# Performance work log

Measured on AMD Instinct MI355X. Metric: run time of the kernel, lower is better.

Reference implementation:

```python
import jax, jax.numpy as jnp
import numpy as np

B, T, F = 8, 8192, 1024
H, O = 256, 2


def setup_inputs() -> dict:
    key = jax.random.key(0)
    ks = jax.random.split(key, 12)
    s = 0.02
    return {
        "bags": jax.random.normal(ks[0], (B, T, F), dtype=jnp.float32),
        "mask": jnp.zeros((B, T), dtype=bool),
        "W1": jax.random.normal(ks[1], (F, H), dtype=jnp.float32) * s,
        "b1": jnp.zeros((H,), dtype=jnp.float32),
        "Wv": jax.random.normal(ks[2], (H, H), dtype=jnp.float32) * s,
        "bv": jnp.zeros((H,), dtype=jnp.float32),
        "Wu": jax.random.normal(ks[3], (H, H), dtype=jnp.float32) * s,
        "bu": jnp.zeros((H,), dtype=jnp.float32),
        "ww": jax.random.normal(ks[4], (H, 1), dtype=jnp.float32) * s,
        "bw": jnp.zeros((1,), dtype=jnp.float32),
        "Wc": jax.random.normal(ks[5], (H, O), dtype=jnp.float32) * s,
        "bc": jnp.zeros((O,), dtype=jnp.float32),
    }


def reference(bags, mask, W1, b1, Wv, bv, Wu, bu, ww, bw, Wc, bc):
    # Feature projection + ReLU (dropout is identity in eval mode)
    h = jax.nn.relu(jnp.einsum("btf,fh->bth", bags, W1) + b1)  # (B,T,H)
    # Gated attention
    a_v = jnp.tanh(jnp.einsum("bth,hk->btk", h, Wv) + bv)
    a_u = jax.nn.sigmoid(jnp.einsum("bth,hk->btk", h, Wu) + bu)
    attn_logits = (jnp.einsum("bth,ho->bto", a_v * a_u, ww) + bw)[..., 0]  # (B,T)
    attn_logits = jnp.where(mask, -jnp.inf, attn_logits)
    attn = jax.nn.softmax(attn_logits, axis=1)  # (B,T)
    # Weighted aggregation over tiles
    slide_repr = jnp.einsum("bt,bth->bh", attn, h)  # (B,H)
    logits = slide_repr @ Wc + bc  # (B,O)
    return logits
```

## Files before the change

### kernel.cpp

```cpp
#include <hip/hip_runtime.h>
#include <math.h>

#define BB 8
#define TT 8192
#define FF 1024
#define HH 256
#define OO 2
#define MT 64
#define NBLK ((BB*TT)/MT)
#define PBAG (TT/MT)
#define PSTR 260

typedef __attribute__((ext_vector_type(8))) short bf16x8;
typedef __attribute__((ext_vector_type(4))) float f32x4;

__device__ __forceinline__ float b2f(unsigned short s) {
    union { unsigned u; float f; } v; v.u = ((unsigned)s) << 16; return v.f;
}
__device__ __forceinline__ unsigned short f2b(float f) {
    union { float f; unsigned u; } v; v.f = f;
    unsigned u = v.u;
    return (unsigned short)((u + 0x7fffu + ((u >> 16) & 1u)) >> 16);
}

__global__ void mil_prep(const float* __restrict__ W1,
                         const float* __restrict__ Wv,
                         const float* __restrict__ Wu,
                         unsigned short* __restrict__ W1t,
                         unsigned short* __restrict__ Wvt,
                         unsigned short* __restrict__ Wut) {
    int i = blockIdx.x;
    int t = threadIdx.x;
    if (i < 1024) {
        W1t[t * 1024 + i] = f2b(W1[i * 256 + t]);
    } else if (i < 1280) {
        int r = i - 1024;
        Wvt[t * 256 + r] = f2b(Wv[r * 256 + t]);
    } else {
        int r = i - 1280;
        Wut[t * 256 + r] = f2b(Wu[r * 256 + t]);
    }
}

__global__ __launch_bounds__(256, 2)
void mil_main(const float* __restrict__ bags,
              const unsigned char* __restrict__ mask,
              const float* __restrict__ b1,
              const float* __restrict__ bv,
              const float* __restrict__ bu,
              const float* __restrict__ ww,
              const float* __restrict__ bwp,
              const unsigned short* __restrict__ W1t,
              const unsigned short* __restrict__ Wvt,
              const unsigned short* __restrict__ Wut,
              float* __restrict__ P) {
    const int tid  = threadIdx.x;
    const int wave = tid >> 6;
    const int lane = tid & 63;
    const int l15  = lane & 15;
    const int quad = lane >> 4;
    const int blk  = blockIdx.x;
    const int row0 = blk * MT;
    const int bag  = blk >> 7;
    const int trow = (blk & 127) * MT;

    __shared__ unsigned short As[MT * 72];
    __shared__ unsigned short Bs[HH * 72];
    __shared__ unsigned short Hs[MT * 264];

    const float bwv = bwp[0];

    f32x4 acc[4][4];
#pragma unroll
    for (int mi = 0; mi < 4; ++mi)
#pragma unroll
        for (int ni = 0; ni < 4; ++ni)
            acc[mi][ni] = (f32x4){0.f, 0.f, 0.f, 0.f};

    const float* bagrow = bags + (size_t)row0 * FF;

    for (int kb = 0; kb < FF / 64; ++kb) {
        __syncthreads();
#pragma unroll
        for (int i = 0; i < 4; ++i) {
            int f = tid + i * 256;
            int r = f >> 4, s = f & 15;
            const float4 v = *(const float4*)(bagrow + (size_t)r * FF + kb * 64 + s * 4);
            unsigned p0 = (unsigned)f2b(v.x) | ((unsigned)f2b(v.y) << 16);
            unsigned p1 = (unsigned)f2b(v.z) | ((unsigned)f2b(v.w) << 16);
            *(uint2*)&As[r * 72 + s * 4] = make_uint2(p0, p1);
        }
#pragma unroll
        for (int i = 0; i < 8; ++i) {
            int f = tid + i * 256;
            int n = f >> 3, s = f & 7;
            *(uint4*)&Bs[n * 72 + s * 8] = *(const uint4*)(W1t + n * 1024 + kb * 64 + s * 8);
        }
        __syncthreads();
#pragma unroll
        for (int k0 = 0; k0 < 64; k0 += 32) {
            bf16x8 af[4], bfr[4];
#pragma unroll
            for (int mi = 0; mi < 4; ++mi)
                af[mi] = *(const bf16x8*)&As[(mi * 16 + l15) * 72 + k0 + quad * 8];
#pragma unroll
            for (int ni = 0; ni < 4; ++ni)
                bfr[ni] = *(const bf16x8*)&Bs[(wave * 64 + ni * 16 + l15) * 72 + k0 + quad * 8];
#pragma unroll
            for (int mi = 0; mi < 4; ++mi)
#pragma unroll
                for (int ni = 0; ni < 4; ++ni)
                    acc[mi][ni] = __builtin_amdgcn_mfma_f32_16x16x32_bf16(af[mi], bfr[ni], acc[mi][ni], 0, 0, 0);
        }
    }

    {
        float bb[4];
#pragma unroll
        for (int ni = 0; ni < 4; ++ni) bb[ni] = b1[wave * 64 + ni * 16 + l15];
#pragma unroll
        for (int mi = 0; mi < 4; ++mi)
#pragma unroll
            for (int ni = 0; ni < 4; ++ni) {
                int n = wave * 64 + ni * 16 + l15;
#pragma unroll
                for (int r = 0; r < 4; ++r) {
                    int m = mi * 16 + quad * 4 + r;
                    float h = acc[mi][ni][r] + bb[ni];
                    h = fmaxf(h, 0.f);
                    Hs[m * 264 + n] = f2b(h);
                }
            }
    }
    __syncthreads();

    float* logits = (float*)As;
    float* wrow   = logits + 64;
    float* sc     = wrow + 64;
    if (tid < MT) logits[tid] = 0.f;

    float gv[4][4][4];
    float rsum[4][4];
#pragma unroll
    for (int mi = 0; mi < 4; ++mi)
#pragma unroll
        for (int r = 0; r < 4; ++r) rsum[mi][r] = 0.f;

    for (int pass = 0; pass < 2; ++pass) {
        const unsigned short* Wt = pass ? Wut : Wvt;
        f32x4 a2[4][4];
#pragma unroll
        for (int mi = 0; mi < 4; ++mi)
#pragma unroll
            for (int ni = 0; ni < 4; ++ni) a2[mi][ni] = (f32x4){0.f, 0.f, 0.f, 0.f};

        for (int kb = 0; kb < HH / 64; ++kb) {
            __syncthreads();
#pragma unroll
            for (int i = 0; i < 8; ++i) {
                int f = tid + i * 256;
                int n = f >> 3, s = f & 7;
                *(uint4*)&Bs[n * 72 + s * 8] = *(const uint4*)(Wt + n * 256 + kb * 64 + s * 8);
            }
            __syncthreads();
#pragma unroll
            for (int k0 = 0; k0 < 64; k0 += 32) {
                int k = kb * 64 + k0 + quad * 8;
                bf16x8 af[4], bfr[4];
#pragma unroll
                for (int mi = 0; mi < 4; ++mi)
                    af[mi] = *(const bf16x8*)&Hs[(mi * 16 + l15) * 264 + k];
#pragma unroll
                for (int ni = 0; ni < 4; ++ni)
                    bfr[ni] = *(const bf16x8*)&Bs[(wave * 64 + ni * 16 + l15) * 72 + k0 + quad * 8];
#pragma unroll
                for (int mi = 0; mi < 4; ++mi)
#pragma unroll
                    for (int ni = 0; ni < 4; ++ni)
                        a2[mi][ni] = __builtin_amdgcn_mfma_f32_16x16x32_bf16(af[mi], bfr[ni], a2[mi][ni], 0, 0, 0);
            }
        }

        if (pass == 0) {
            float bb[4];
#pragma unroll
            for (int ni = 0; ni < 4; ++ni) bb[ni] = bv[wave * 64 + ni * 16 + l15];
#pragma unroll
            for (int mi = 0; mi < 4; ++mi)
#pragma unroll
                for (int ni = 0; ni < 4; ++ni)
#pragma unroll
                    for (int r = 0; r < 4; ++r)
                        gv[mi][ni][r] = tanhf(a2[mi][ni][r] + bb[ni]);
        } else {
            float bb[4], wn[4];
#pragma unroll
            for (int ni = 0; ni < 4; ++ni) {
                int n = wave * 64 + ni * 16 + l15;
                bb[ni] = bu[n];
                wn[ni] = ww[n];
            }
#pragma unroll
            for (int mi = 0; mi < 4; ++mi)
#pragma unroll
                for (int ni = 0; ni < 4; ++ni)
#pragma unroll
                    for (int r = 0; r < 4; ++r) {
                        float su = 1.f / (1.f + expf(-(a2[mi][ni][r] + bb[ni])));
                        rsum[mi][r] += gv[mi][ni][r] * su * wn[ni];
                    }
#pragma unroll
            for (int mi = 0; mi < 4; ++mi)
#pragma unroll
                for (int r = 0; r < 4; ++r) {
                    float s = rsum[mi][r];
                    s += __shfl_xor(s, 1);
                    s += __shfl_xor(s, 2);
                    s += __shfl_xor(s, 4);
                    s += __shfl_xor(s, 8);
                    if (l15 == 0) atomicAdd(&logits[mi * 16 + quad * 4 + r], s);
                }
        }
    }
    __syncthreads();

    if (tid < MT) {
        float lg = logits[tid] + bwv;
        if (mask[bag * TT + trow + tid]) lg = -INFINITY;
        logits[tid] = lg;
    }
    __syncthreads();

    if (wave == 0) {
        float v = logits[lane];
        float mx = v;
#pragma unroll
        for (int off = 1; off < 64; off <<= 1) mx = fmaxf(mx, __shfl_xor(mx, off));
        float w = (mx == -INFINITY) ? 0.f : expf(v - mx);
        wrow[lane] = w;
        float l = w;
#pragma unroll
        for (int off = 1; off < 64; off <<= 1) l += __shfl_xor(l, off);
        if (lane == 0) { sc[0] = mx; sc[1] = l; }
    }
    __syncthreads();

    float a = 0.f;
#pragma unroll 8
    for (int m = 0; m < MT; ++m)
        a += wrow[m] * b2f(Hs[m * 264 + tid]);

    float* rec = P + (size_t)blk * PSTR;
    rec[2 + tid] = a;
    if (tid == 0) { rec[0] = sc[0]; rec[1] = sc[1]; }
}

__global__ void mil_final(const float* __restrict__ P,
                          const float* __restrict__ Wc,
                          const float* __restrict__ bc,
                          float* __restrict__ out) {
    const int bag = blockIdx.x;
    const int tid = threadIdx.x;
    __shared__ float marr[PBAG];
    __shared__ float earr[PBAG];
    __shared__ float slide[HH];
    __shared__ float wred[8];
    __shared__ float sM, sL;

    if (tid < PBAG) marr[tid] = P[(size_t)(bag * PBAG + tid) * PSTR + 0];
    __syncthreads();
    if (tid == 0) {
        float M = -INFINITY;
        for (int i = 0; i < PBAG; ++i) M = fmaxf(M, marr[i]);
        sM = M;
    }
    __syncthreads();
    const float M = sM;
    if (tid < PBAG) {
        float e = (marr[tid] == -INFINITY) ? 0.f : expf(marr[tid] - M);
        earr[tid] = e;
        marr[tid] = P[(size_t)(bag * PBAG + tid) * PSTR + 1] * e;
    }
    __syncthreads();
    if (tid == 0) {
        float L = 0.f;
        for (int i = 0; i < PBAG; ++i) L += marr[i];
        sL = L;
    }
    __syncthreads();
    const float L = sL;

    float accv = 0.f;
    for (int i = 0; i < PBAG; ++i)
        accv += earr[i] * P[(size_t)(bag * PBAG + i) * PSTR + 2 + tid];
    slide[tid] = accv / L;
    __syncthreads();

    float p0 = slide[tid] * Wc[tid * 2 + 0];
    float p1 = slide[tid] * Wc[tid * 2 + 1];
#pragma unroll
    for (int off = 1; off < 64; off <<= 1) {
        p0 += __shfl_xor(p0, off);
        p1 += __shfl_xor(p1, off);
    }
    if ((tid & 63) == 0) {
        wred[(tid >> 6) * 2 + 0] = p0;
        wred[(tid >> 6) * 2 + 1] = p1;
    }
    __syncthreads();
    if (tid == 0) {
        out[bag * 2 + 0] = wred[0] + wred[2] + wred[4] + wred[6] + bc[0];
        out[bag * 2 + 1] = wred[1] + wred[3] + wred[5] + wred[7] + bc[1];
    }
}

extern "C" void kernel_launch(void* const* d_in, const int* in_sizes, int n_in,
                              void* d_out, int out_size, void* d_ws, size_t ws_size,
                              hipStream_t stream) {
    const float*         bags = (const float*)d_in[0];
    const unsigned char* mask = (const unsigned char*)d_in[1];
    const float*         W1   = (const float*)d_in[2];
    const float*         b1   = (const float*)d_in[3];
    const float*         Wv   = (const float*)d_in[4];
    const float*         bv   = (const float*)d_in[5];
    const float*         Wu   = (const float*)d_in[6];
    const float*         bu   = (const float*)d_in[7];
    const float*         ww   = (const float*)d_in[8];
    const float*         bw   = (const float*)d_in[9];
    const float*         Wc   = (const float*)d_in[10];
    const float*         bc   = (const float*)d_in[11];
    float* out = (float*)d_out;

    char* ws = (char*)d_ws;
    unsigned short* W1t = (unsigned short*)(ws);
    unsigned short* Wvt = (unsigned short*)(ws + 524288);
    unsigned short* Wut = (unsigned short*)(ws + 655360);
    float*          P   = (float*)(ws + 786432);

    mil_prep<<<1536, 256, 0, stream>>>(W1, Wv, Wu, W1t, Wvt, Wut);
    mil_main<<<NBLK, 256, 0, stream>>>(bags, mask, b1, bv, bu, ww, bw, W1t, Wvt, Wut, P);
    mil_final<<<BB, 256, 0, stream>>>(P, Wc, bc, out);
}
```

Measured before the change: 461.8 us.

## Stream weights from global, prefetch bag tiles, fuse gate GEMMs, tile weight transpose

The main kernel stops staging W1/Wv/Wu through shared memory. Each wave now loads its B fragments straight from global memory, which is mostly L2-resident. Freeing the large Bs buffer lets occupancy go to three blocks per CU, and the next bag tile is register-prefetched while the current one is computed. The Wv and Wu GEMMs are fused into a single pass over the hidden state, so the gv register array disappears. The weight prep kernel becomes a tiled, coalesced transpose, and the final kernel replaces its serial reductions with wave shuffles. The trade-off is more global and L2 traffic for weight fragments and added register pressure from the prefetch buffers.

```diff
diff --git a/kernel.cpp b/kernel.cpp
--- a/kernel.cpp
+++ b/kernel.cpp
@@ -23,26 +23,43 @@
     return (unsigned short)((u + 0x7fffu + ((u >> 16) & 1u)) >> 16);
 }
 
-__global__ void mil_prep(const float* __restrict__ W1,
-                         const float* __restrict__ Wv,
-                         const float* __restrict__ Wu,
-                         unsigned short* __restrict__ W1t,
-                         unsigned short* __restrict__ Wvt,
-                         unsigned short* __restrict__ Wut) {
-    int i = blockIdx.x;
-    int t = threadIdx.x;
-    if (i < 1024) {
-        W1t[t * 1024 + i] = f2b(W1[i * 256 + t]);
-    } else if (i < 1280) {
-        int r = i - 1024;
-        Wvt[t * 256 + r] = f2b(Wv[r * 256 + t]);
-    } else {
-        int r = i - 1280;
-        Wut[t * 256 + r] = f2b(Wu[r * 256 + t]);
-    }
-}
-
-__global__ __launch_bounds__(256, 2)
+__global__ __launch_bounds__(256)
+void mil_prep(const float* __restrict__ W1,
+              const float* __restrict__ Wv,
+              const float* __restrict__ Wu,
+              unsigned short* __restrict__ W1t,
+              unsigned short* __restrict__ Wvt,
+              unsigned short* __restrict__ Wut) {
+    __shared__ unsigned short T[64 * 72];
+    const int b = blockIdx.x;
+    const int t = threadIdx.x;
+    const float* src;
+    unsigned short* dst;
+    int kt, nt, dstld;
+    if (b < 64)      { src = W1; dst = W1t; kt = b >> 2;        nt = b & 3;        dstld = 1024; }
+    else if (b < 80) { src = Wv; dst = Wvt; kt = (b - 64) >> 2; nt = (b - 64) & 3; dstld = 256; }
+    else             { src = Wu; dst = Wut; kt = (b - 80) >> 2; nt = (b - 80) & 3; dstld = 256; }
+
+#pragma unroll
+    for (int i = 0; i < 4; ++i) {
+        int f = t + i * 256;
+        int r = f >> 4, c = (f & 15) * 4;
+        float4 v = *(const float4*)(src + (size_t)(kt * 64 + r) * 256 + nt * 64 + c);
+        T[(c + 0) * 72 + r] = f2b(v.x);
+        T[(c + 1) * 72 + r] = f2b(v.y);
+        T[(c + 2) * 72 + r] = f2b(v.z);
+        T[(c + 3) * 72 + r] = f2b(v.w);
+    }
+    __syncthreads();
+#pragma unroll
+    for (int i = 0; i < 2; ++i) {
+        int f = t + i * 256;
+        int r = f >> 3, s = (f & 7) * 8;
+        *(uint4*)(dst + (size_t)(nt * 64 + r) * dstld + kt * 64 + s) = *(uint4*)&T[r * 72 + s];
+    }
+}
+
+__global__ __launch_bounds__(256, 3)
 void mil_main(const float* __restrict__ bags,
               const unsigned char* __restrict__ mask,
               const float* __restrict__ b1,
@@ -65,7 +82,6 @@
     const int trow = (blk & 127) * MT;
 
     __shared__ unsigned short As[MT * 72];
-    __shared__ unsigned short Bs[HH * 72];
     __shared__ unsigned short Hs[MT * 264];
 
     const float bwv = bwp[0];
@@ -79,38 +95,48 @@
 
     const float* bagrow = bags + (size_t)row0 * FF;
 
+    float4 pf[4];
+    int pr[4], pc[4];
+#pragma unroll
+    for (int i = 0; i < 4; ++i) {
+        int f = tid + i * 256;
+        pr[i] = f >> 4;
+        pc[i] = (f & 15) * 4;
+        pf[i] = *(const float4*)(bagrow + (size_t)pr[i] * FF + pc[i]);
+    }
+
     for (int kb = 0; kb < FF / 64; ++kb) {
         __syncthreads();
 #pragma unroll
         for (int i = 0; i < 4; ++i) {
-            int f = tid + i * 256;
-            int r = f >> 4, s = f & 15;
-            const float4 v = *(const float4*)(bagrow + (size_t)r * FF + kb * 64 + s * 4);
-            unsigned p0 = (unsigned)f2b(v.x) | ((unsigned)f2b(v.y) << 16);
-            unsigned p1 = (unsigned)f2b(v.z) | ((unsigned)f2b(v.w) << 16);
-            *(uint2*)&As[r * 72 + s * 4] = make_uint2(p0, p1);
-        }
-#pragma unroll
-        for (int i = 0; i < 8; ++i) {
-            int f = tid + i * 256;
-            int n = f >> 3, s = f & 7;
-            *(uint4*)&Bs[n * 72 + s * 8] = *(const uint4*)(W1t + n * 1024 + kb * 64 + s * 8);
+            unsigned p0 = (unsigned)f2b(pf[i].x) | ((unsigned)f2b(pf[i].y) << 16);
+            unsigned p1 = (unsigned)f2b(pf[i].z) | ((unsigned)f2b(pf[i].w) << 16);
+            *(uint2*)&As[pr[i] * 72 + pc[i]] = make_uint2(p0, p1);
         }
         __syncthreads();
-#pragma unroll
-        for (int k0 = 0; k0 < 64; k0 += 32) {
-            bf16x8 af[4], bfr[4];
-#pragma unroll
-            for (int mi = 0; mi < 4; ++mi)
-                af[mi] = *(const bf16x8*)&As[(mi * 16 + l15) * 72 + k0 + quad * 8];
+        bf16x8 bfr[2][4];
+#pragma unroll
+        for (int k0i = 0; k0i < 2; ++k0i)
 #pragma unroll
             for (int ni = 0; ni < 4; ++ni)
-                bfr[ni] = *(const bf16x8*)&Bs[(wave * 64 + ni * 16 + l15) * 72 + k0 + quad * 8];
+                bfr[k0i][ni] = *(const bf16x8*)(W1t + (size_t)(wave * 64 + ni * 16 + l15) * 1024
+                                                + kb * 64 + k0i * 32 + quad * 8);
+        if (kb < FF / 64 - 1) {
+#pragma unroll
+            for (int i = 0; i < 4; ++i)
+                pf[i] = *(const float4*)(bagrow + (size_t)pr[i] * FF + (kb + 1) * 64 + pc[i]);
+        }
+#pragma unroll
+        for (int k0i = 0; k0i < 2; ++k0i) {
+            bf16x8 afr[4];
+#pragma unroll
+            for (int mi = 0; mi < 4; ++mi)
+                afr[mi] = *(const bf16x8*)&As[(mi * 16 + l15) * 72 + k0i * 32 + quad * 8];
 #pragma unroll
             for (int mi = 0; mi < 4; ++mi)
 #pragma unroll
                 for (int ni = 0; ni < 4; ++ni)
-                    acc[mi][ni] = __builtin_amdgcn_mfma_f32_16x16x32_bf16(af[mi], bfr[ni], acc[mi][ni], 0, 0, 0);
+                    acc[mi][ni] = __builtin_amdgcn_mfma_f32_16x16x32_bf16(afr[mi], bfr[k0i][ni], acc[mi][ni], 0, 0, 0);
         }
     }
 
@@ -138,90 +164,71 @@
     float* wrow   = logits + 64;
     float* sc     = wrow + 64;
     if (tid < MT) logits[tid] = 0.f;
-
-    float gv[4][4][4];
+    __syncthreads();
+
     float rsum[4][4];
 #pragma unroll
     for (int mi = 0; mi < 4; ++mi)
 #pragma unroll
         for (int r = 0; r < 4; ++r) rsum[mi][r] = 0.f;
 
-    for (int pass = 0; pass < 2; ++pass) {
-        const unsigned short* Wt = pass ? Wut : Wvt;
-        f32x4 a2[4][4];
+#pragma unroll
+    for (int nc = 0; nc < 2; ++nc) {
+        f32x4 av[4][2], au[4][2];
 #pragma unroll
         for (int mi = 0; mi < 4; ++mi)
 #pragma unroll
-            for (int ni = 0; ni < 4; ++ni) a2[mi][ni] = (f32x4){0.f, 0.f, 0.f, 0.f};
-
-        for (int kb = 0; kb < HH / 64; ++kb) {
-            __syncthreads();
-#pragma unroll
-            for (int i = 0; i < 8; ++i) {
-                int f = tid + i * 256;
-                int n = f >> 3, s = f & 7;
-                *(uint4*)&Bs[n * 72 + s * 8] = *(const uint4*)(Wt + n * 256 + kb * 64 + s * 8);
+            for (int j = 0; j < 2; ++j) {
+                av[mi][j] = (f32x4){0.f, 0.f, 0.f, 0.f};
+                au[mi][j] = (f32x4){0.f, 0.f, 0.f, 0.f};
             }
-            __syncthreads();
-#pragma unroll
-            for (int k0 = 0; k0 < 64; k0 += 32) {
-                int k = kb * 64 + k0 + quad * 8;
-                bf16x8 af[4], bfr[4];
-#pragma unroll
-                for (int mi = 0; mi < 4; ++mi)
-                    af[mi] = *(const bf16x8*)&Hs[(mi * 16 + l15) * 264 + k];
-#pragma unroll
-                for (int ni = 0; ni < 4; ++ni)
-                    bfr[ni] = *(const bf16x8*)&Bs[(wave * 64 + ni * 16 + l15) * 72 + k0 + quad * 8];
-#pragma unroll
-                for (int mi = 0; mi < 4; ++mi)
-#pragma unroll
-                    for (int ni = 0; ni < 4; ++ni)
-                        a2[mi][ni] = __builtin_amdgcn_mfma_f32_16x16x32_bf16(af[mi], bfr[ni], a2[mi][ni], 0, 0, 0);
+#pragma unroll 2
+        for (int ks = 0; ks < 8; ++ks) {
+            int k = ks * 32 + quad * 8;
+            bf16x8 bvf[2], buf[2];
+#pragma unroll
+            for (int j = 0; j < 2; ++j) {
+                int n = wave * 64 + (nc * 2 + j) * 16 + l15;
+                bvf[j] = *(const bf16x8*)(Wvt + (size_t)n * 256 + k);
+                buf[j] = *(const bf16x8*)(Wut + (size_t)n * 256 + k);
             }
-        }
-
-        if (pass == 0) {
-            float bb[4];
-#pragma unroll
-            for (int ni = 0; ni < 4; ++ni) bb[ni] = bv[wave * 64 + ni * 16 + l15];
-#pragma unroll
-            for (int mi = 0; mi < 4; ++mi)
-#pragma unroll
-                for (int ni = 0; ni < 4; ++ni)
-#pragma unroll
-                    for (int r = 0; r < 4; ++r)
-                        gv[mi][ni][r] = tanhf(a2[mi][ni][r] + bb[ni]);
-        } else {
-            float bb[4], wn[4];
-#pragma unroll
-            for (int ni = 0; ni < 4; ++ni) {
-                int n = wave * 64 + ni * 16 + l15;
-                bb[ni] = bu[n];
-                wn[ni] = ww[n];
-            }
-#pragma unroll
-            for (int mi = 0; mi < 4; ++mi)
-#pragma unroll
-                for (int ni = 0; ni < 4; ++ni)
-#pragma unroll
-                    for (int r = 0; r < 4; ++r) {
-                        float su = 1.f / (1.f + expf(-(a2[mi][ni][r] + bb[ni])));
-                        rsum[mi][r] += gv[mi][ni][r] * su * wn[ni];
-                    }
+            bf16x8 afr[4];
+#pragma unroll
+            for (int mi = 0; mi < 4; ++mi)
+                afr[mi] = *(const bf16x8*)&Hs[(mi * 16 + l15) * 264 + k];
+#pragma unroll
+            for (int mi = 0; mi < 4; ++mi)
+#pragma unroll
+                for (int j = 0; j < 2; ++j) {
+                    av[mi][j] = __builtin_amdgcn_mfma_f32_16x16x32_bf16(afr[mi], bvf[j], av[mi][j], 0, 0, 0);
+                    au[mi][j] = __builtin_amdgcn_mfma_f32_16x16x32_bf16(afr[mi], buf[j], au[mi][j], 0, 0, 0);
+                }
+        }
+#pragma unroll
+        for (int j = 0; j < 2; ++j) {
+            int n = wave * 64 + (nc * 2 + j) * 16 + l15;
+            float bvn = bv[n], bun = bu[n], wn = ww[n];
 #pragma unroll
             for (int mi = 0; mi < 4; ++mi)
 #pragma unroll
                 for (int r = 0; r < 4; ++r) {
-                    float s = rsum[mi][r];
-                    s += __shfl_xor(s, 1);
-                    s += __shfl_xor(s, 2);
-                    s += __shfl_xor(s, 4);
-                    s += __shfl_xor(s, 8);
-                    if (l15 == 0) atomicAdd(&logits[mi * 16 + quad * 4 + r], s);
+                    float tv = tanhf(av[mi][j][r] + bvn);
+                    float su = 1.f / (1.f + expf(-(au[mi][j][r] + bun)));
+                    rsum[mi][r] += tv * su * wn;
                 }
         }
     }
+#pragma unroll
+    for (int mi = 0; mi < 4; ++mi)
+#pragma unroll
+        for (int r = 0; r < 4; ++r) {
+            float s = rsum[mi][r];
+            s += __shfl_xor(s, 1);
+            s += __shfl_xor(s, 2);
+            s += __shfl_xor(s, 4);
+            s += __shfl_xor(s, 8);
+            if (l15 == 0) atomicAdd(&logits[mi * 16 + quad * 4 + r], s);
+        }
     __syncthreads();
 
     if (tid < MT) {
@@ -263,41 +270,37 @@
     const int tid = threadIdx.x;
     __shared__ float marr[PBAG];
     __shared__ float earr[PBAG];
-    __shared__ float slide[HH];
+    __shared__ float red[4];
     __shared__ float wred[8];
-    __shared__ float sM, sL;
 
     if (tid < PBAG) marr[tid] = P[(size_t)(bag * PBAG + tid) * PSTR + 0];
     __syncthreads();
-    if (tid == 0) {
-        float M = -INFINITY;
-        for (int i = 0; i < PBAG; ++i) M = fmaxf(M, marr[i]);
-        sM = M;
-    }
-    __syncthreads();
-    const float M = sM;
+    if (tid < PBAG) {
+        float v = marr[tid];
+#pragma unroll
+        for (int off = 1; off < 64; off <<= 1) v = fmaxf(v, __shfl_xor(v, off));
+        if ((tid & 63) == 0) red[tid >> 6] = v;
+    }
+    __syncthreads();
+    const float M = fmaxf(red[0], red[1]);
     if (tid < PBAG) {
         float e = (marr[tid] == -INFINITY) ? 0.f : expf(marr[tid] - M);
         earr[tid] = e;
-        marr[tid] = P[(size_t)(bag * PBAG + tid) * PSTR + 1] * e;
-    }
-    __syncthreads();
-    if (tid == 0) {
-        float L = 0.f;
-        for (int i = 0; i < PBAG; ++i) L += marr[i];
-        sL = L;
-    }
-    __syncthreads();
-    const float L = sL;
+        float le = P[(size_t)(bag * PBAG + tid) * PSTR + 1] * e;
+#pragma unroll
+        for (int off = 1; off < 64; off <<= 1) le += __shfl_xor(le, off);
+        if ((tid & 63) == 0) red[2 + (tid >> 6)] = le;
+    }
+    __syncthreads();
+    const float L = red[2] + red[3];
 
     float accv = 0.f;
     for (int i = 0; i < PBAG; ++i)
         accv += earr[i] * P[(size_t)(bag * PBAG + i) * PSTR + 2 + tid];
-    slide[tid] = accv / L;
-    __syncthreads();
-
-    float p0 = slide[tid] * Wc[tid * 2 + 0];
-    float p1 = slide[tid] * Wc[tid * 2 + 1];
+    const float sr = accv / L;
+
+    float p0 = sr * Wc[tid * 2 + 0];
+    float p1 = sr * Wc[tid * 2 + 1];
 #pragma unroll
     for (int off = 1; off < 64; off <<= 1) {
         p0 += __shfl_xor(p0, off);
@@ -337,7 +340,7 @@
     unsigned short* Wut = (unsigned short*)(ws + 655360);
     float*          P   = (float*)(ws + 786432);
 
-    mil_prep<<<1536, 256, 0, stream>>>(W1, Wv, Wu, W1t, Wvt, Wut);
+    mil_prep<<<96, 256, 0, stream>>>(W1, Wv, Wu, W1t, Wvt, Wut);
     mil_main<<<NBLK, 256, 0, stream>>>(bags, mask, b1, bv, bu, ww, bw, W1t, Wvt, Wut, P);
     mil_final<<<BB, 256, 0, stream>>>(P, Wc, bc, out);
 }
```

Result: slower. 496.7 us (+7.5%).
